# Performance work log

Measured on AMD Instinct MI355X. Metric: run time of the kernel, lower is better.

## Reference

```python
import jax, jax.numpy as jnp
import numpy as np

N_NODES = 50000
N_EDGES = 600000
NUM_RELS = 5
IN_CH = 768
HID = 128
OUT_CH = 128
REL_DIM = 200


def _segment_softmax(scores, seg, n):
    # numerically stable softmax over variable-size segments (destination nodes)
    m = jax.ops.segment_max(scores, seg, num_segments=n)
    e = jnp.exp(scores - m[seg])
    s = jax.ops.segment_sum(e, seg, num_segments=n)
    return e / s[seg]


def _hgn_conv(x, edge_index, edge_type, W, Wr, a, Wres, rel_tab, final):
    # x: [N, h_in]; W: [h, h_in]; Wr: [h, rel_dim]; a: [3h]; rel_tab: [R, rel_dim]
    src = edge_index[0]
    dst = edge_index[1]
    n = x.shape[0]
    h = W.shape[0]
    Wx = x @ W.T                      # [N, h] (shared by x_i, x_j, messages)
    rel = rel_tab[edge_type] @ Wr.T   # [E, h]
    aA, aB, aC = a[:h], a[h:2 * h], a[2 * h:]
    # a([Wx_i | Wx_j | Wr rel]) decomposed to avoid materializing the concat
    score = Wx[dst] @ aA + Wx[src] @ aB + rel @ aC   # [E]
    alpha = jax.nn.leaky_relu(score, 0.2)
    alpha = _segment_softmax(alpha, dst, n)
    agg = jax.ops.segment_sum(Wx[src] * alpha[:, None], dst, num_segments=n)
    out = jax.nn.elu(agg + x @ Wres.T)
    if final:
        out = out / jnp.maximum(jnp.linalg.norm(out, axis=1, keepdims=True), 1e-12)
    return out, alpha


def setup_inputs() -> dict:
    key = jax.random.key(0)
    ks = jax.random.split(key, 20)
    s = 0.02
    return {
        "x": jax.random.normal(ks[0], (N_NODES, IN_CH), jnp.float32),
        "edge_index": jax.random.randint(ks[1], (2, N_EDGES), 0, N_NODES, jnp.int64 if jax.config.jax_enable_x64 else jnp.int32),
        "edge_type": jax.random.randint(ks[2], (N_EDGES,), 0, NUM_RELS, jnp.int64 if jax.config.jax_enable_x64 else jnp.int32),
        "l1_W": jax.random.normal(ks[3], (HID, IN_CH), jnp.float32) * s,
        "l1_b": jnp.zeros((HID,), jnp.float32),
        "l2_W": jax.random.normal(ks[4], (OUT_CH, HID), jnp.float32) * s,
        "l2_b": jnp.zeros((OUT_CH,), jnp.float32),
        "W1": jax.random.normal(ks[5], (HID, HID), jnp.float32) * s,
        "Wr1": jax.random.normal(ks[6], (HID, REL_DIM), jnp.float32) * s,
        "a1": jax.random.normal(ks[7], (3 * HID,), jnp.float32) * s,
        "Wres1": jax.random.normal(ks[8], (HID, HID), jnp.float32) * s,
        "rel1": jax.random.normal(ks[9], (NUM_RELS, REL_DIM), jnp.float32),
        "W2": jax.random.normal(ks[10], (HID, HID), jnp.float32) * s,
        "Wr2": jax.random.normal(ks[11], (HID, REL_DIM), jnp.float32) * s,
        "a2": jax.random.normal(ks[12], (3 * HID,), jnp.float32) * s,
        "Wres2": jax.random.normal(ks[13], (HID, HID), jnp.float32) * s,
        "rel2": jax.random.normal(ks[14], (NUM_RELS, REL_DIM), jnp.float32),
    }


def reference(x, edge_index, edge_type, l1_W, l1_b, l2_W, l2_b,
              W1, Wr1, a1, Wres1, rel1, W2, Wr2, a2, Wres2, rel2):
    out = jax.nn.leaky_relu(x @ l1_W.T + l1_b, 0.01)
    # layer 1 (dropout is identity in eval mode)
    out, alpha = _hgn_conv(out, edge_index, edge_type, W1, Wr1, a1, Wres1, rel1, final=False)
    # layer 2: original code blends alpha into self.alpha but weights messages
    # with its own (unblended) softmax alpha, so pre_alpha does not affect output
    out, _ = _hgn_conv(out, edge_index, edge_type, W2, Wr2, a2, Wres2, rel2, final=True)
    out = jax.nn.leaky_relu(out @ l2_W.T + l2_b, 0.01)
    return out
```

## Files before the change

### kernel.cpp

```cpp
#include <hip/hip_runtime.h>

namespace {

typedef unsigned short ushort_t;
typedef unsigned int uint_t;
typedef __attribute__((ext_vector_type(8))) short bf16x8;
typedef __attribute__((ext_vector_type(4))) float f32x4;

constexpr int N   = 50000;
constexpr int E   = 600000;
constexpr int NR  = 5;
constexpr int KIN = 768;
constexpr int H   = 128;
constexpr int RD  = 200;

__device__ inline ushort_t f2b(float f){
  uint_t u = __builtin_bit_cast(uint_t, f);
  uint_t r = (u + 0x7FFFu + ((u >> 16) & 1u)) >> 16;
  return (ushort_t)r;
}
__device__ inline float b2f_lo(uint_t u){ return __builtin_bit_cast(float, u << 16); }
__device__ inline float b2f_hi(uint_t u){ return __builtin_bit_cast(float, u & 0xFFFF0000u); }
__device__ inline float b2f_us(ushort_t h){ return __builtin_bit_cast(float, ((uint_t)h) << 16); }
__device__ inline uint_t cvtpk(float lo, float hi){
  uint_t r;
  asm("v_cvt_pk_bf16_f32 %0, %1, %2" : "=v"(r) : "v"(lo), "v"(hi));
  return r;
}

__global__ void prep_k(const float* __restrict__ l1W, const float* __restrict__ W1,
                       const float* __restrict__ R1, const float* __restrict__ W2,
                       const float* __restrict__ R2, const float* __restrict__ l2W,
                       ushort_t* __restrict__ wts, int* __restrict__ deg,
                       const float* __restrict__ rel1, const float* __restrict__ Wr1,
                       const float* __restrict__ a1, float* __restrict__ sC1,
                       const float* __restrict__ rel2, const float* __restrict__ Wr2,
                       const float* __restrict__ a2, float* __restrict__ sC2){
  constexpr int S0 = H * KIN;
  constexpr int S1 = H * H;
  int b = blockIdx.x, tid = threadIdx.x;
  if (b < 704){
    int i = b * 256 + tid;
    float v;
    if (i < S0) v = l1W[i];
    else {
      int j = i - S0, seg = j >> 14, off = j & (S1 - 1);
      const float* srcs[5] = {W1, R1, W2, R2, l2W};
      v = srcs[seg][off];
    }
    wts[i] = f2b(v);
  } else if (b < 900){
    int i = (b - 704) * 256 + tid;
    if (i < N) deg[i] = 0;
  } else {
    int L = b - 900;
    const float* rel = L ? rel2 : rel1;
    const float* Wr  = L ? Wr2  : Wr1;
    const float* a   = L ? a2   : a1;
    float*       sC  = L ? sC2  : sC1;
    __shared__ float red[256];
    int n = tid >> 1, half = tid & 1;
    float aC = a[256 + n];
    for (int r = 0; r < NR; ++r){
      float p = 0.f;
      for (int k = half * 100; k < half * 100 + 100; ++k)
        p += rel[r * RD + k] * Wr[n * RD + k];
      red[tid] = p * aC;
      __syncthreads();
      for (int s = 128; s > 0; s >>= 1){
        if (tid < s) red[tid] += red[tid + s];
        __syncthreads();
      }
      if (tid == 0) sC[r] = red[0];
      __syncthreads();
    }
  }
}

__global__ void degcount_k(const int* __restrict__ dst, int* __restrict__ deg){
  int e = blockIdx.x * 256 + threadIdx.x;
  if (e < E) atomicAdd(&deg[dst[e]], 1);
}

__global__ void scan1_k(const int* __restrict__ deg, int* __restrict__ chunk,
                        int* __restrict__ bsums, int n){
  __shared__ int s[256];
  int tid = threadIdx.x, i = blockIdx.x * 256 + tid;
  int v = (i < n) ? deg[i] : 0;
  s[tid] = v; __syncthreads();
  for (int off = 1; off < 256; off <<= 1){
    int t = (tid >= off) ? s[tid - off] : 0;
    __syncthreads();
    s[tid] += t;
    __syncthreads();
  }
  if (i < n) chunk[i] = s[tid] - v;
  if (tid == 255) bsums[blockIdx.x] = s[255];
}

__global__ void scan2_k(const int* __restrict__ bsums, int* __restrict__ boffs, int nb){
  __shared__ int s[256];
  int tid = threadIdx.x;
  int v = (tid < nb) ? bsums[tid] : 0;
  s[tid] = v; __syncthreads();
  for (int off = 1; off < 256; off <<= 1){
    int t = (tid >= off) ? s[tid - off] : 0;
    __syncthreads();
    s[tid] += t;
    __syncthreads();
  }
  if (tid < nb) boffs[tid] = s[tid] - v;
}

__global__ void scan3_k(int* __restrict__ rowptr, const int* __restrict__ boffs,
                        int* __restrict__ cursor, int n, int total){
  int i = blockIdx.x * 256 + threadIdx.x;
  if (i < n){
    int v = rowptr[i] + boffs[blockIdx.x];
    rowptr[i] = v; cursor[i] = v;
  }
  if (i == 0) rowptr[n] = total;
}

__global__ void fill_k(const int* __restrict__ src, const int* __restrict__ dst,
                       const int* __restrict__ et, int* __restrict__ cursor,
                       int* __restrict__ cpk){
  int e = blockIdx.x * 256 + threadIdx.x;
  if (e < E){
    int d = dst[e];
    int p = atomicAdd(&cursor[d], 1);
    cpk[p] = src[e] | (et[e] << 16);
  }
}

template<int K1, int M1, bool AFP32, bool NORM, bool STORE1, int M2>
__global__ __launch_bounds__(256, 3) void gfused_k(
    const void* __restrict__ Ap, const ushort_t* __restrict__ Wb1,
    const float* __restrict__ bias1, const ushort_t* __restrict__ aggM,
    ushort_t* __restrict__ out1,
    const ushort_t* __restrict__ Wb2, const float* __restrict__ vec2,
    void* __restrict__ out2, float* __restrict__ sA, float* __restrict__ sB, int M)
{
  __shared__ __align__(16) ushort_t Cs[64 * 128];
  const int tid  = threadIdx.x;
  const int wave = tid >> 6, lane = tid & 63;
  const int l15  = lane & 15, quad = lane >> 4;
  const int row0 = blockIdx.x * 64;
  const int arow_l = wave * 16 + l15;
  int ar = row0 + arow_l; if (ar >= M) ar = M - 1;

  f32x4 acc[8];
  #pragma unroll
  for (int t = 0; t < 8; ++t) acc[t] = (f32x4){0.f, 0.f, 0.f, 0.f};

  const ushort_t* wb = Wb1 + (size_t)l15 * K1 + quad * 8;
  if (AFP32){
    const float* ap = (const float*)Ap + (size_t)ar * K1 + quad * 8;
    #pragma unroll 2
    for (int k0 = 0; k0 < K1; k0 += 32){
      float4 u0 = *reinterpret_cast<const float4*>(ap + k0);
      float4 u1 = *reinterpret_cast<const float4*>(ap + k0 + 4);
      uint4 av;
      av.x = cvtpk(u0.x, u0.y); av.y = cvtpk(u0.z, u0.w);
      av.z = cvtpk(u1.x, u1.y); av.w = cvtpk(u1.z, u1.w);
      bf16x8 af = __builtin_bit_cast(bf16x8, av);
      #pragma unroll
      for (int t = 0; t < 8; ++t){
        bf16x8 bfr = *reinterpret_cast<const bf16x8*>(wb + (size_t)t * 16 * K1 + k0);
        acc[t] = __builtin_amdgcn_mfma_f32_16x16x32_bf16(af, bfr, acc[t], 0, 0, 0);
      }
    }
  } else {
    const ushort_t* apb = (const ushort_t*)Ap + (size_t)ar * K1 + quad * 8;
    #pragma unroll 2
    for (int k0 = 0; k0 < K1; k0 += 32){
      bf16x8 af = *reinterpret_cast<const bf16x8*>(apb + k0);
      #pragma unroll
      for (int t = 0; t < 8; ++t){
        bf16x8 bfr = *reinterpret_cast<const bf16x8*>(wb + (size_t)t * 16 * K1 + k0);
        acc[t] = __builtin_amdgcn_mfma_f32_16x16x32_bf16(af, bfr, acc[t], 0, 0, 0);
      }
    }
  }

  const int lr0 = wave * 16 + quad * 4;
  float vv[8][4];
  #pragma unroll
  for (int t = 0; t < 8; ++t){
    #pragma unroll
    for (int r = 0; r < 4; ++r){
      int col = t * 16 + l15;
      float v = acc[t][r];
      if (M1 == 1){
        v += bias1[col];
        v = v > 0.f ? v : 0.01f * v;
      } else {
        int g = row0 + lr0 + r;
        float ag = (g < M) ? b2f_us(aggM[(size_t)g * 128 + col]) : 0.f;
        v += ag;
        v = v > 0.f ? v : __expf(v) - 1.f;
      }
      vv[t][r] = v;
    }
  }
  if (NORM){
    #pragma unroll
    for (int r = 0; r < 4; ++r){
      float ss = 0.f;
      #pragma unroll
      for (int t = 0; t < 8; ++t) ss += vv[t][r] * vv[t][r];
      #pragma unroll
      for (int off = 1; off < 16; off <<= 1) ss += __shfl_xor(ss, off, 64);
      float sc = 1.f / fmaxf(sqrtf(ss), 1e-12f);
      #pragma unroll
      for (int t = 0; t < 8; ++t) vv[t][r] *= sc;
    }
  }
  #pragma unroll
  for (int t = 0; t < 8; t += 2){
    #pragma unroll
    for (int r = 0; r < 4; ++r){
      int row = lr0 + r;
      int key = row & 7;
      uint_t pr = cvtpk(vv[t][r], vv[t + 1][r]);
      int c0 = t * 16 + l15, c1 = c0 + 16;
      int p0 = ((c0 >> 3) ^ key) << 3, p1 = ((c1 >> 3) ^ key) << 3;
      Cs[row * 128 + p0 + (l15 & 7)] = (ushort_t)pr;
      Cs[row * 128 + p1 + (l15 & 7)] = (ushort_t)(pr >> 16);
      if (STORE1){
        int g = row0 + row;
        if (g < M){
          out1[(size_t)g * 128 + c0] = (ushort_t)pr;
          out1[(size_t)g * 128 + c1] = (ushort_t)(pr >> 16);
        }
      }
    }
  }
  __syncthreads();

  #pragma unroll
  for (int t = 0; t < 8; ++t) acc[t] = (f32x4){0.f, 0.f, 0.f, 0.f};
  {
    const int rr   = wave * 16 + l15;
    const int rkey = l15 & 7;
    const ushort_t* w2 = Wb2 + (size_t)l15 * 128 + quad * 8;
    #pragma unroll 2
    for (int kk = 0; kk < 4; ++kk){
      int ph = (((kk * 4 + quad) ^ rkey) << 3);
      bf16x8 af2 = *reinterpret_cast<const bf16x8*>(&Cs[rr * 128 + ph]);
      #pragma unroll
      for (int t = 0; t < 8; ++t){
        bf16x8 bfr = *reinterpret_cast<const bf16x8*>(w2 + (size_t)t * 16 * 128 + kk * 32);
        acc[t] = __builtin_amdgcn_mfma_f32_16x16x32_bf16(af2, bfr, acc[t], 0, 0, 0);
      }
    }
  }

  if (M2 == 1){
    #pragma unroll
    for (int t = 0; t < 8; ++t){
      #pragma unroll
      for (int r = 0; r < 4; ++r){
        int grow = row0 + lr0 + r;
        if (grow >= M) continue;
        int col = t * 16 + l15;
        float v = acc[t][r] + vec2[col];
        v = v > 0.f ? v : 0.01f * v;
        ((float*)out2)[(size_t)grow * 128 + col] = v;
      }
    }
  } else {
    #pragma unroll
    for (int t = 0; t < 8; t += 2){
      #pragma unroll
      for (int r = 0; r < 4; ++r){
        int grow = row0 + lr0 + r;
        if (grow >= M) continue;
        int c0 = t * 16 + l15;
        uint_t pr = cvtpk(acc[t][r], acc[t + 1][r]);
        ((ushort_t*)out2)[(size_t)grow * 128 + c0]      = (ushort_t)pr;
        ((ushort_t*)out2)[(size_t)grow * 128 + c0 + 16] = (ushort_t)(pr >> 16);
      }
    }
    #pragma unroll
    for (int r = 0; r < 4; ++r){
      float pa = 0.f, pb = 0.f;
      #pragma unroll
      for (int t = 0; t < 8; ++t){
        int col = t * 16 + l15;
        pa += acc[t][r] * vec2[col];
        pb += acc[t][r] * vec2[128 + col];
      }
      #pragma unroll
      for (int off = 1; off < 16; off <<= 1){
        pa += __shfl_xor(pa, off, 64);
        pb += __shfl_xor(pb, off, 64);
      }
      int grow = row0 + lr0 + r;
      if (l15 == r && grow < M){ sA[grow] = pa; sB[grow] = pb; }
    }
  }
}

__global__ __launch_bounds__(256) void agg_k(
    const ushort_t* __restrict__ Wx, const float* __restrict__ sA,
    const float* __restrict__ sB, const float* __restrict__ sC,
    const int* __restrict__ rowptr, const int* __restrict__ cpk,
    uint_t* __restrict__ aggU, int n)
{
  const int node  = blockIdx.x * 16 + (threadIdx.x >> 4);
  const int l     = threadIdx.x & 15;
  const int gbase = threadIdx.x & 48;
  if (node >= n) return;
  int p0 = rowptr[node], p1 = rowptr[node + 1];
  int deg = p1 - p0;
  float sa = sA[node];
  float m = -1e30f, ssum = 0.f;
  float a[8];
  #pragma unroll
  for (int j = 0; j < 8; ++j) a[j] = 0.f;

  for (int c0 = 0; c0 < deg; c0 += 16){
    int cnt = deg - c0; if (cnt > 16) cnt = 16;
    bool ok = l < cnt;
    int pk = cpk[p0 + c0 + (ok ? l : 0)];
    float s = sa + sB[pk & 0xFFFF] + sC[pk >> 16];
    s = s > 0.f ? s : 0.2f * s;
    float sv = ok ? s : -1e30f;
    #pragma unroll
    for (int off = 8; off > 0; off >>= 1) sv = fmaxf(sv, __shfl_xor(sv, off, 16));
    float mn = fmaxf(m, sv);
    float corr = __expf(m - mn);
    ssum *= corr;
    #pragma unroll
    for (int j = 0; j < 8; ++j) a[j] *= corr;
    float ev = ok ? __expf(s - mn) : 0.f;
    float es = ev;
    #pragma unroll
    for (int off = 8; off > 0; off >>= 1) es += __shfl_xor(es, off, 16);
    ssum += es;
    m = mn;
    int png = ok ? pk : 0;

    for (int e = 0; e < cnt; e += 4){
      int b0l = gbase + e;
      int pe0 = __shfl(png, b0l,     64), pe1 = __shfl(png, b0l + 1, 64);
      int pe2 = __shfl(png, b0l + 2, 64), pe3 = __shfl(png, b0l + 3, 64);
      float e0 = __shfl(ev, b0l,     64), e1 = __shfl(ev, b0l + 1, 64);
      float e2 = __shfl(ev, b0l + 2, 64), e3 = __shfl(ev, b0l + 3, 64);
      uint4 u0 = *reinterpret_cast<const uint4*>(Wx + (size_t)(pe0 & 0xFFFF) * 128 + l * 8);
      uint4 u1 = *reinterpret_cast<const uint4*>(Wx + (size_t)(pe1 & 0xFFFF) * 128 + l * 8);
      uint4 u2 = *reinterpret_cast<const uint4*>(Wx + (size_t)(pe2 & 0xFFFF) * 128 + l * 8);
      uint4 u3 = *reinterpret_cast<const uint4*>(Wx + (size_t)(pe3 & 0xFFFF) * 128 + l * 8);
      a[0] += e0 * b2f_lo(u0.x); a[1] += e0 * b2f_hi(u0.x);
      a[2] += e0 * b2f_lo(u0.y); a[3] += e0 * b2f_hi(u0.y);
      a[4] += e0 * b2f_lo(u0.z); a[5] += e0 * b2f_hi(u0.z);
      a[6] += e0 * b2f_lo(u0.w); a[7] += e0 * b2f_hi(u0.w);
      a[0] += e1 * b2f_lo(u1.x); a[1] += e1 * b2f_hi(u1.x);
      a[2] += e1 * b2f_lo(u1.y); a[3] += e1 * b2f_hi(u1.y);
      a[4] += e1 * b2f_lo(u1.z); a[5] += e1 * b2f_hi(u1.z);
      a[6] += e1 * b2f_lo(u1.w); a[7] += e1 * b2f_hi(u1.w);
      a[0] += e2 * b2f_lo(u2.x); a[1] += e2 * b2f_hi(u2.x);
      a[2] += e2 * b2f_lo(u2.y); a[3] += e2 * b2f_hi(u2.y);
      a[4] += e2 * b2f_lo(u2.z); a[5] += e2 * b2f_hi(u2.z);
      a[6] += e2 * b2f_lo(u2.w); a[7] += e2 * b2f_hi(u2.w);
      a[0] += e3 * b2f_lo(u3.x); a[1] += e3 * b2f_hi(u3.x);
      a[2] += e3 * b2f_lo(u3.y); a[3] += e3 * b2f_hi(u3.y);
      a[4] += e3 * b2f_lo(u3.z); a[5] += e3 * b2f_hi(u3.z);
      a[6] += e3 * b2f_lo(u3.w); a[7] += e3 * b2f_hi(u3.w);
    }
  }
  float inv = (deg > 0) ? 1.f / ssum : 0.f;
  uint4 o;
  o.x = cvtpk(a[0] * inv, a[1] * inv);
  o.y = cvtpk(a[2] * inv, a[3] * inv);
  o.z = cvtpk(a[4] * inv, a[5] * inv);
  o.w = cvtpk(a[6] * inv, a[7] * inv);
  *reinterpret_cast<uint4*>(aggU + (size_t)node * 64 + l * 4) = o;
}

}

extern "C" void kernel_launch(void* const* d_in, const int* in_sizes, int n_in,
                              void* d_out, int out_size, void* d_ws, size_t ws_size,
                              hipStream_t stream)
{
  const float* x     = (const float*)d_in[0];
  const int*   eidx  = (const int*)d_in[1];
  const int*   et    = (const int*)d_in[2];
  const float* l1W   = (const float*)d_in[3];
  const float* l1b   = (const float*)d_in[4];
  const float* l2W   = (const float*)d_in[5];
  const float* l2b   = (const float*)d_in[6];
  const float* W1    = (const float*)d_in[7];
  const float* Wr1   = (const float*)d_in[8];
  const float* a1    = (const float*)d_in[9];
  const float* Wres1 = (const float*)d_in[10];
  const float* rel1  = (const float*)d_in[11];
  const float* W2    = (const float*)d_in[12];
  const float* Wr2   = (const float*)d_in[13];
  const float* a2    = (const float*)d_in[14];
  const float* Wres2 = (const float*)d_in[15];
  const float* rel2  = (const float*)d_in[16];
  float* outp = (float*)d_out;

  const int* esrc = eidx;
  const int* edst = eidx + E;

  float* f = (float*)d_ws;
  size_t o = 0;
  float* sA   = f + o; o += N;
  float* sB   = f + o; o += N;
  float* sC1  = f + o; o += 8;
  float* sC2  = f + o; o += 8;
  ushort_t* us = (ushort_t*)(f + o);
  size_t ou = 0;
  ushort_t* b0   = us + ou; ou += (size_t)N * H;
  ushort_t* b1   = us + ou; ou += (size_t)N * H;
  ushort_t* Wxb  = us + ou; ou += (size_t)N * H;
  ushort_t* aggB = us + ou; ou += (size_t)N * H;
  ushort_t* wtsb = us + ou; ou += (size_t)H * KIN + 5 * H * H;
  ushort_t* l1Wb = wtsb;
  ushort_t* W1b  = wtsb + H * KIN;
  ushort_t* R1b  = W1b + H * H;
  ushort_t* W2b  = R1b + H * H;
  ushort_t* R2b  = W2b + H * H;
  ushort_t* l2Wb = R2b + H * H;
  if (ou & 1) ou += 1;
  int* wi = (int*)(us + ou);
  size_t oi = 0;
  int* deg    = wi + oi; oi += N;
  int* rowptr = wi + oi; oi += N + 1;
  int* cursor = wi + oi; oi += N;
  int* bsums  = wi + oi; oi += 256;
  int* boffs  = wi + oi; oi += 256;
  int* cpk    = wi + oi; oi += E;

  const int EB    = (E + 255) / 256;
  const int NB256 = (N + 255) / 256;
  const int GB    = (N + 63) / 64;
  const int NB16  = (N + 15) / 16;

  prep_k<<<902, 256, 0, stream>>>(l1W, W1, Wres1, W2, Wres2, l2W, wtsb, deg,
                                  rel1, Wr1, a1, sC1, rel2, Wr2, a2, sC2);
  degcount_k<<<EB, 256, 0, stream>>>(edst, deg);
  scan1_k<<<NB256, 256, 0, stream>>>(deg, rowptr, bsums, N);
  scan2_k<<<1, 256, 0, stream>>>(bsums, boffs, NB256);
  scan3_k<<<NB256, 256, 0, stream>>>(rowptr, boffs, cursor, N, E);
  fill_k<<<EB, 256, 0, stream>>>(esrc, edst, et, cursor, cpk);

  gfused_k<KIN, 1, true, false, true, 3><<<GB, 256, 0, stream>>>(
      x, l1Wb, l1b, nullptr, b0, W1b, a1, Wxb, sA, sB, N);
  agg_k<<<NB16, 256, 0, stream>>>(Wxb, sA, sB, sC1, rowptr, cpk, (uint_t*)aggB, N);

  gfused_k<H, 2, false, false, true, 3><<<GB, 256, 0, stream>>>(
      b0, R1b, nullptr, aggB, b1, W2b, a2, Wxb, sA, sB, N);
  agg_k<<<NB16, 256, 0, stream>>>(Wxb, sA, sB, sC2, rowptr, cpk, (uint_t*)aggB, N);

  gfused_k<H, 2, false, true, false, 1><<<GB, 256, 0, stream>>>(
      b1, R2b, nullptr, aggB, nullptr, l2Wb, l2b, outp, nullptr, nullptr, N);
}
```

Before: 575.2 us.

## Stage GEMM A/B tiles through LDS with async global_load_lds pipelining

Rewrites the first GEMM main loop in the fused kernel. Instead of every wave loading A and B fragments straight from global memory, the A tiles are double-buffered in LDS (converted to bf16 on the way in) and the weight B tiles are triple-buffered in LDS using global_load_lds, with explicit vmcnt waits and barriers so loads overlap the MFMAs. It also stages the aggregated aggM tile into LDS with coalesced 16-byte loads instead of scattered 2-byte reads. The costs are more LDS per block, which may limit occupancy at 3 blocks per CU, and hand-tuned waitcnt logic that is fragile.

```diff
diff --git a/kernel.cpp b/kernel.cpp
--- a/kernel.cpp
+++ b/kernel.cpp
@@ -26,6 +26,18 @@
   uint_t r;
   asm("v_cvt_pk_bf16_f32 %0, %1, %2" : "=v"(r) : "v"(lo), "v"(hi));
   return r;
+}
+
+typedef __attribute__((address_space(1))) const unsigned int glb_u32;
+typedef __attribute__((address_space(3))) unsigned int lds_u32;
+__device__ __forceinline__ void glds16(const void* g, void* l){
+  __builtin_amdgcn_global_load_lds((glb_u32*)g, (lds_u32*)l, 16, 0, 0);
+}
+template<int Nn> __device__ __forceinline__ void wait_vmcnt(){
+  asm volatile("s_waitcnt vmcnt(%0)" :: "n"(Nn) : "memory");
+}
+__device__ __forceinline__ void wait_lgkm0(){
+  asm volatile("s_waitcnt lgkmcnt(0)" ::: "memory");
 }
 
 __global__ void prep_k(const float* __restrict__ l1W, const float* __restrict__ W1,
@@ -141,46 +153,109 @@
     const ushort_t* __restrict__ Wb2, const float* __restrict__ vec2,
     void* __restrict__ out2, float* __restrict__ sA, float* __restrict__ sB, int M)
 {
+  constexpr int NT = K1 / 32;
+  constexpr int AI = AFP32 ? 2 : 1;
+  __shared__ __align__(16) ushort_t Abuf[2][64 * 32];
+  __shared__ __align__(16) ushort_t Bbuf[3][128 * 32];
   __shared__ __align__(16) ushort_t Cs[64 * 128];
   const int tid  = threadIdx.x;
   const int wave = tid >> 6, lane = tid & 63;
   const int l15  = lane & 15, quad = lane >> 4;
   const int row0 = blockIdx.x * 64;
-  const int arow_l = wave * 16 + l15;
-  int ar = row0 + arow_l; if (ar >= M) ar = M - 1;
+
+  int arow_ld = row0 + (tid >> 2); if (arow_ld >= M) arow_ld = M - 1;
+  const int aoff  = (tid & 3) * 8;
+  const int awoff = (tid >> 2) * 32 + aoff;
+  const int c0 = wave * 2, c1 = wave * 2 + 1;
+  const ushort_t* bsrc0 = Wb1 + (size_t)(c0 * 16 + (lane >> 2)) * K1 + (lane & 3) * 8;
+  const ushort_t* bsrc1 = bsrc0 + (size_t)16 * K1;
+
+#define ISSUE_A(d0, d1, kk) do{                                               \
+    if constexpr (AFP32){                                                     \
+      const float* ap_ = (const float*)Ap + (size_t)arow_ld * K1 + (kk) + aoff; \
+      d0 = *reinterpret_cast<const uint4*>(ap_);                              \
+      d1 = *reinterpret_cast<const uint4*>(ap_ + 4);                          \
+    } else {                                                                  \
+      d0 = *reinterpret_cast<const uint4*>(                                   \
+          (const ushort_t*)Ap + (size_t)arow_ld * K1 + (kk) + aoff);          \
+    } }while(0)
+
+#define WRITE_A(bi, s0, s1) do{ uint4 av_;                                    \
+    if constexpr (AFP32){                                                     \
+      float4 f0_ = __builtin_bit_cast(float4, s0);                            \
+      float4 f1_ = __builtin_bit_cast(float4, s1);                            \
+      av_.x = cvtpk(f0_.x, f0_.y); av_.y = cvtpk(f0_.z, f0_.w);               \
+      av_.z = cvtpk(f1_.x, f1_.y); av_.w = cvtpk(f1_.z, f1_.w);               \
+    } else av_ = s0;                                                          \
+    *reinterpret_cast<uint4*>(&Abuf[bi][awoff]) = av_; }while(0)
+
+#define ISSUE_B(bi, kk) do{                                                   \
+    glds16(bsrc0 + (kk), &Bbuf[bi][c0 * 512]);                                \
+    glds16(bsrc1 + (kk), &Bbuf[bi][c1 * 512]); }while(0)
+
+#define KSTEP(ab, bb) do{                                                     \
+    bf16x8 af_ = *reinterpret_cast<const bf16x8*>(                            \
+        &Abuf[ab][(wave * 16 + l15) * 32 + quad * 8]);                        \
+    _Pragma("unroll")                                                         \
+    for (int t_ = 0; t_ < 8; ++t_){                                           \
+      bf16x8 bf_ = *reinterpret_cast<const bf16x8*>(                          \
+          &Bbuf[bb][(t_ * 16 + l15) * 32 + quad * 8]);                        \
+      acc[t_] = __builtin_amdgcn_mfma_f32_16x16x32_bf16(af_, bf_, acc[t_], 0, 0, 0); \
+    } }while(0)
 
   f32x4 acc[8];
   #pragma unroll
   for (int t = 0; t < 8; ++t) acc[t] = (f32x4){0.f, 0.f, 0.f, 0.f};
 
-  const ushort_t* wb = Wb1 + (size_t)l15 * K1 + quad * 8;
-  if (AFP32){
-    const float* ap = (const float*)Ap + (size_t)ar * K1 + quad * 8;
-    #pragma unroll 2
-    for (int k0 = 0; k0 < K1; k0 += 32){
-      float4 u0 = *reinterpret_cast<const float4*>(ap + k0);
-      float4 u1 = *reinterpret_cast<const float4*>(ap + k0 + 4);
-      uint4 av;
-      av.x = cvtpk(u0.x, u0.y); av.y = cvtpk(u0.z, u0.w);
-      av.z = cvtpk(u1.x, u1.y); av.w = cvtpk(u1.z, u1.w);
-      bf16x8 af = __builtin_bit_cast(bf16x8, av);
-      #pragma unroll
-      for (int t = 0; t < 8; ++t){
-        bf16x8 bfr = *reinterpret_cast<const bf16x8*>(wb + (size_t)t * 16 * K1 + k0);
-        acc[t] = __builtin_amdgcn_mfma_f32_16x16x32_bf16(af, bfr, acc[t], 0, 0, 0);
-      }
-    }
-  } else {
-    const ushort_t* apb = (const ushort_t*)Ap + (size_t)ar * K1 + quad * 8;
-    #pragma unroll 2
-    for (int k0 = 0; k0 < K1; k0 += 32){
-      bf16x8 af = *reinterpret_cast<const bf16x8*>(apb + k0);
-      #pragma unroll
-      for (int t = 0; t < 8; ++t){
-        bf16x8 bfr = *reinterpret_cast<const bf16x8*>(wb + (size_t)t * 16 * K1 + k0);
-        acc[t] = __builtin_amdgcn_mfma_f32_16x16x32_bf16(af, bfr, acc[t], 0, 0, 0);
-      }
-    }
+  uint4 pa0_0, pa0_1, pa1_0, pa1_1;
+  ISSUE_A(pa0_0, pa0_1, 0);
+  ISSUE_B(0, 0);
+  ISSUE_A(pa1_0, pa1_1, 32);
+  ISSUE_B(1, 32);
+  wait_vmcnt<AI + 4>();
+  WRITE_A(0, pa0_0, pa0_1);
+  wait_lgkm0();
+  __builtin_amdgcn_s_barrier();
+
+  int bt = 0;
+  for (int t = 0; t < NT; t += 2){
+    wait_vmcnt<AI + 2>();
+    KSTEP(0, bt);
+    wait_vmcnt<2>();
+    WRITE_A(1, pa1_0, pa1_1);
+    { int b2 = bt + 2; if (b2 >= 3) b2 -= 3;
+      if (t + 2 < NT){ ISSUE_A(pa0_0, pa0_1, (t + 2) * 32); ISSUE_B(b2, (t + 2) * 32); } }
+    wait_lgkm0();
+    __builtin_amdgcn_s_barrier();
+    bt = (bt >= 2) ? 0 : bt + 1;
+    wait_vmcnt<AI + 2>();
+    KSTEP(1, bt);
+    if (t + 2 < NT){
+      wait_vmcnt<2>();
+      WRITE_A(0, pa0_0, pa0_1);
+    }
+    { int b2 = bt + 2; if (b2 >= 3) b2 -= 3;
+      if (t + 3 < NT){ ISSUE_A(pa1_0, pa1_1, (t + 3) * 32); ISSUE_B(b2, (t + 3) * 32); } }
+    wait_lgkm0();
+    __builtin_amdgcn_s_barrier();
+    bt = (bt >= 2) ? 0 : bt + 1;
+  }
+#undef ISSUE_A
+#undef WRITE_A
+#undef ISSUE_B
+#undef KSTEP
+
+  ushort_t* Ag = &Bbuf[0][0];
+  if (M1 == 2){
+    #pragma unroll
+    for (int i = 0; i < 4; ++i){
+      int idx = tid + 256 * i, r = idx >> 4, c8 = idx & 15;
+      int g = row0 + r;
+      uint4 v = make_uint4(0, 0, 0, 0);
+      if (g < M) v = *reinterpret_cast<const uint4*>(aggM + (size_t)g * 128 + c8 * 8);
+      *reinterpret_cast<uint4*>(&Ag[r * 128 + c8 * 8]) = v;
+    }
+    __syncthreads();
   }
 
   const int lr0 = wave * 16 + quad * 4;
@@ -195,9 +270,7 @@
         v += bias1[col];
         v = v > 0.f ? v : 0.01f * v;
       } else {
-        int g = row0 + lr0 + r;
-        float ag = (g < M) ? b2f_us(aggM[(size_t)g * 128 + col]) : 0.f;
-        v += ag;
+        v += b2f_us(Ag[(lr0 + r) * 128 + col]);
         v = v > 0.f ? v : __expf(v) - 1.f;
       }
       vv[t][r] = v;
@@ -223,15 +296,15 @@
       int row = lr0 + r;
       int key = row & 7;
       uint_t pr = cvtpk(vv[t][r], vv[t + 1][r]);
-      int c0 = t * 16 + l15, c1 = c0 + 16;
-      int p0 = ((c0 >> 3) ^ key) << 3, p1 = ((c1 >> 3) ^ key) << 3;
+      int c0s = t * 16 + l15, c1s = c0s + 16;
+      int p0 = ((c0s >> 3) ^ key) << 3, p1 = ((c1s >> 3) ^ key) << 3;
       Cs[row * 128 + p0 + (l15 & 7)] = (ushort_t)pr;
       Cs[row * 128 + p1 + (l15 & 7)] = (ushort_t)(pr >> 16);
       if (STORE1){
         int g = row0 + row;
         if (g < M){
-          out1[(size_t)g * 128 + c0] = (ushort_t)pr;
-          out1[(size_t)g * 128 + c1] = (ushort_t)(pr >> 16);
+          out1[(size_t)g * 128 + c0s] = (ushort_t)pr;
+          out1[(size_t)g * 128 + c1s] = (ushort_t)(pr >> 16);
         }
       }
     }
@@ -276,10 +349,10 @@
       for (int r = 0; r < 4; ++r){
         int grow = row0 + lr0 + r;
         if (grow >= M) continue;
-        int c0 = t * 16 + l15;
+        int c0s = t * 16 + l15;
         uint_t pr = cvtpk(acc[t][r], acc[t + 1][r]);
-        ((ushort_t*)out2)[(size_t)grow * 128 + c0]      = (ushort_t)pr;
-        ((ushort_t*)out2)[(size_t)grow * 128 + c0 + 16] = (ushort_t)(pr >> 16);
+        ((ushort_t*)out2)[(size_t)grow * 128 + c0s]      = (ushort_t)pr;
+        ((ushort_t*)out2)[(size_t)grow * 128 + c0s + 16] = (ushort_t)(pr >> 16);
       }
     }
     #pragma unroll
```

After: 524.1 us. 8.9% less time.

## Stage GEMM tiles in LDS with register prefetch and 2x2 wave split

Applied to the files above, without the earlier changes.

The fused GEMM kernel now processes 32-row blocks split across a 2x2 wave grid, each wave computing 16 rows by 64 columns. A and W tiles are staged through padded shared memory with a one-step register prefetch, instead of each wave reading W fragments straight from global memory. The aggregate input is preloaded into shared memory, and the norm and score reductions are combined across the two column-waves through a small shared buffer. Launch bounds allow higher occupancy, at the cost of two barriers per K step and twice as many blocks.

```diff
diff --git a/kernel.cpp b/kernel.cpp
--- a/kernel.cpp
+++ b/kernel.cpp
@@ -134,70 +134,92 @@
 }
 
 template<int K1, int M1, bool AFP32, bool NORM, bool STORE1, int M2>
-__global__ __launch_bounds__(256, 3) void gfused_k(
+__global__ __launch_bounds__(256, 6) void gfused_k(
     const void* __restrict__ Ap, const ushort_t* __restrict__ Wb1,
     const float* __restrict__ bias1, const ushort_t* __restrict__ aggM,
     ushort_t* __restrict__ out1,
     const ushort_t* __restrict__ Wb2, const float* __restrict__ vec2,
     void* __restrict__ out2, float* __restrict__ sA, float* __restrict__ sB, int M)
 {
-  __shared__ __align__(16) ushort_t Cs[64 * 128];
+  constexpr int AP = 40;
+  constexpr int BP = 40;
+  constexpr int CP = 136;
+  __shared__ __align__(16) ushort_t As[32 * AP];
+  __shared__ __align__(16) ushort_t Bs[128 * BP];
+  __shared__ __align__(16) ushort_t Cs[32 * CP];
+  __shared__ float cmb[2][32][2];
   const int tid  = threadIdx.x;
   const int wave = tid >> 6, lane = tid & 63;
   const int l15  = lane & 15, quad = lane >> 4;
-  const int row0 = blockIdx.x * 64;
-  const int arow_l = wave * 16 + l15;
-  int ar = row0 + arow_l; if (ar >= M) ar = M - 1;
-
-  f32x4 acc[8];
+  const int wr   = wave >> 1, wc = wave & 1;
+  const int row0 = blockIdx.x * 32;
+
+  if (M1 == 2){
+    #pragma unroll
+    for (int i = 0; i < 2; ++i){
+      int idx = tid + 256 * i;
+      int r = idx >> 4, c8 = idx & 15;
+      int g = row0 + r;
+      uint4 v = make_uint4(0, 0, 0, 0);
+      if (g < M) v = *reinterpret_cast<const uint4*>(aggM + (size_t)g * 128 + c8 * 8);
+      *reinterpret_cast<uint4*>(&Cs[r * CP + c8 * 8]) = v;
+    }
+  }
+
+  f32x4 acc[4];
   #pragma unroll
-  for (int t = 0; t < 8; ++t) acc[t] = (f32x4){0.f, 0.f, 0.f, 0.f};
-
-  const ushort_t* wb = Wb1 + (size_t)l15 * K1 + quad * 8;
-  if (AFP32){
-    const float* ap = (const float*)Ap + (size_t)ar * K1 + quad * 8;
-    #pragma unroll 2
-    for (int k0 = 0; k0 < K1; k0 += 32){
-      float4 u0 = *reinterpret_cast<const float4*>(ap + k0);
-      float4 u1 = *reinterpret_cast<const float4*>(ap + k0 + 4);
-      uint4 av;
-      av.x = cvtpk(u0.x, u0.y); av.y = cvtpk(u0.z, u0.w);
-      av.z = cvtpk(u1.x, u1.y); av.w = cvtpk(u1.z, u1.w);
-      bf16x8 af = __builtin_bit_cast(bf16x8, av);
-      #pragma unroll
-      for (int t = 0; t < 8; ++t){
-        bf16x8 bfr = *reinterpret_cast<const bf16x8*>(wb + (size_t)t * 16 * K1 + k0);
-        acc[t] = __builtin_amdgcn_mfma_f32_16x16x32_bf16(af, bfr, acc[t], 0, 0, 0);
-      }
-    }
-  } else {
-    const ushort_t* apb = (const ushort_t*)Ap + (size_t)ar * K1 + quad * 8;
-    #pragma unroll 2
-    for (int k0 = 0; k0 < K1; k0 += 32){
-      bf16x8 af = *reinterpret_cast<const bf16x8*>(apb + k0);
-      #pragma unroll
-      for (int t = 0; t < 8; ++t){
-        bf16x8 bfr = *reinterpret_cast<const bf16x8*>(wb + (size_t)t * 16 * K1 + k0);
-        acc[t] = __builtin_amdgcn_mfma_f32_16x16x32_bf16(af, bfr, acc[t], 0, 0, 0);
-      }
-    }
-  }
-
-  const int lr0 = wave * 16 + quad * 4;
-  float vv[8][4];
+  for (int t = 0; t < 4; ++t) acc[t] = (f32x4){0.f, 0.f, 0.f, 0.f};
+
+  const int arow_s = tid >> 3, aseg = tid & 7;
+  int agrow = row0 + arow_s; if (agrow >= M) agrow = M - 1;
+  const int awoff = arow_s * AP + aseg * 4;
+  const int bn = tid >> 1, bs16 = (tid & 1) * 16;
+  const ushort_t* bsrc = Wb1 + (size_t)bn * K1 + bs16;
+
+  float4 pfa; uint2 pua; uint4 pb0, pb1;
+  if (AFP32) pfa = *reinterpret_cast<const float4*>((const float*)Ap + (size_t)agrow * K1 + aseg * 4);
+  else       pua = *reinterpret_cast<const uint2*>((const ushort_t*)Ap + (size_t)agrow * K1 + aseg * 4);
+  pb0 = *reinterpret_cast<const uint4*>(bsrc);
+  pb1 = *reinterpret_cast<const uint4*>(bsrc + 8);
+
+  for (int k0 = 0; k0 < K1; k0 += 32){
+    { uint2 w;
+      if (AFP32){ w.x = cvtpk(pfa.x, pfa.y); w.y = cvtpk(pfa.z, pfa.w); }
+      else w = pua;
+      *reinterpret_cast<uint2*>(&As[awoff]) = w;
+      *reinterpret_cast<uint4*>(&Bs[bn * BP + bs16])     = pb0;
+      *reinterpret_cast<uint4*>(&Bs[bn * BP + bs16 + 8]) = pb1;
+    }
+    __syncthreads();
+    if (k0 + 32 < K1){
+      const int k1 = k0 + 32;
+      if (AFP32) pfa = *reinterpret_cast<const float4*>((const float*)Ap + (size_t)agrow * K1 + k1 + aseg * 4);
+      else       pua = *reinterpret_cast<const uint2*>((const ushort_t*)Ap + (size_t)agrow * K1 + k1 + aseg * 4);
+      pb0 = *reinterpret_cast<const uint4*>(bsrc + k1);
+      pb1 = *reinterpret_cast<const uint4*>(bsrc + k1 + 8);
+    }
+    bf16x8 af = *reinterpret_cast<const bf16x8*>(&As[(wr * 16 + l15) * AP + quad * 8]);
+    #pragma unroll
+    for (int t = 0; t < 4; ++t){
+      bf16x8 bfr = *reinterpret_cast<const bf16x8*>(&Bs[(wc * 64 + t * 16 + l15) * BP + quad * 8]);
+      acc[t] = __builtin_amdgcn_mfma_f32_16x16x32_bf16(af, bfr, acc[t], 0, 0, 0);
+    }
+    __syncthreads();
+  }
+
+  const int lr0 = wr * 16 + quad * 4;
+  float vv[4][4];
   #pragma unroll
-  for (int t = 0; t < 8; ++t){
+  for (int t = 0; t < 4; ++t){
     #pragma unroll
     for (int r = 0; r < 4; ++r){
-      int col = t * 16 + l15;
+      int col = wc * 64 + t * 16 + l15;
       float v = acc[t][r];
       if (M1 == 1){
         v += bias1[col];
         v = v > 0.f ? v : 0.01f * v;
       } else {
-        int g = row0 + lr0 + r;
-        float ag = (g < M) ? b2f_us(aggM[(size_t)g * 128 + col]) : 0.f;
-        v += ag;
+        v += b2f_us(Cs[(lr0 + r) * CP + col]);
         v = v > 0.f ? v : __expf(v) - 1.f;
       }
       vv[t][r] = v;
@@ -208,25 +230,29 @@
     for (int r = 0; r < 4; ++r){
       float ss = 0.f;
       #pragma unroll
-      for (int t = 0; t < 8; ++t) ss += vv[t][r] * vv[t][r];
+      for (int t = 0; t < 4; ++t) ss += vv[t][r] * vv[t][r];
       #pragma unroll
       for (int off = 1; off < 16; off <<= 1) ss += __shfl_xor(ss, off, 64);
-      float sc = 1.f / fmaxf(sqrtf(ss), 1e-12f);
-      #pragma unroll
-      for (int t = 0; t < 8; ++t) vv[t][r] *= sc;
+      if (l15 == 0) cmb[wc][lr0 + r][0] = ss;
+    }
+    __syncthreads();
+    #pragma unroll
+    for (int r = 0; r < 4; ++r){
+      float tot = cmb[0][lr0 + r][0] + cmb[1][lr0 + r][0];
+      float sc = 1.f / fmaxf(sqrtf(tot), 1e-12f);
+      #pragma unroll
+      for (int t = 0; t < 4; ++t) vv[t][r] *= sc;
     }
   }
   #pragma unroll
-  for (int t = 0; t < 8; t += 2){
+  for (int t = 0; t < 4; t += 2){
     #pragma unroll
     for (int r = 0; r < 4; ++r){
       int row = lr0 + r;
-      int key = row & 7;
+      int c0 = wc * 64 + t * 16 + l15, c1 = c0 + 16;
       uint_t pr = cvtpk(vv[t][r], vv[t + 1][r]);
-      int c0 = t * 16 + l15, c1 = c0 + 16;
-      int p0 = ((c0 >> 3) ^ key) << 3, p1 = ((c1 >> 3) ^ key) << 3;
-      Cs[row * 128 + p0 + (l15 & 7)] = (ushort_t)pr;
-      Cs[row * 128 + p1 + (l15 & 7)] = (ushort_t)(pr >> 16);
+      Cs[row * CP + c0] = (ushort_t)pr;
+      Cs[row * CP + c1] = (ushort_t)(pr >> 16);
       if (STORE1){
         int g = row0 + row;
         if (g < M){
@@ -239,17 +265,15 @@
   __syncthreads();
 
   #pragma unroll
-  for (int t = 0; t < 8; ++t) acc[t] = (f32x4){0.f, 0.f, 0.f, 0.f};
+  for (int t = 0; t < 4; ++t) acc[t] = (f32x4){0.f, 0.f, 0.f, 0.f};
   {
-    const int rr   = wave * 16 + l15;
-    const int rkey = l15 & 7;
-    const ushort_t* w2 = Wb2 + (size_t)l15 * 128 + quad * 8;
-    #pragma unroll 2
+    const int rr = wr * 16 + l15;
+    const ushort_t* w2 = Wb2 + (size_t)(wc * 64 + l15) * 128 + quad * 8;
+    #pragma unroll
     for (int kk = 0; kk < 4; ++kk){
-      int ph = (((kk * 4 + quad) ^ rkey) << 3);
-      bf16x8 af2 = *reinterpret_cast<const bf16x8*>(&Cs[rr * 128 + ph]);
-      #pragma unroll
-      for (int t = 0; t < 8; ++t){
+      bf16x8 af2 = *reinterpret_cast<const bf16x8*>(&Cs[rr * CP + kk * 32 + quad * 8]);
+      #pragma unroll
+      for (int t = 0; t < 4; ++t){
         bf16x8 bfr = *reinterpret_cast<const bf16x8*>(w2 + (size_t)t * 16 * 128 + kk * 32);
         acc[t] = __builtin_amdgcn_mfma_f32_16x16x32_bf16(af2, bfr, acc[t], 0, 0, 0);
       }
@@ -258,12 +282,12 @@
 
   if (M2 == 1){
     #pragma unroll
-    for (int t = 0; t < 8; ++t){
+    for (int t = 0; t < 4; ++t){
       #pragma unroll
       for (int r = 0; r < 4; ++r){
         int grow = row0 + lr0 + r;
         if (grow >= M) continue;
-        int col = t * 16 + l15;
+        int col = wc * 64 + t * 16 + l15;
         float v = acc[t][r] + vec2[col];
         v = v > 0.f ? v : 0.01f * v;
         ((float*)out2)[(size_t)grow * 128 + col] = v;
@@ -271,12 +295,12 @@
     }
   } else {
     #pragma unroll
-    for (int t = 0; t < 8; t += 2){
+    for (int t = 0; t < 4; t += 2){
       #pragma unroll
       for (int r = 0; r < 4; ++r){
         int grow = row0 + lr0 + r;
         if (grow >= M) continue;
-        int c0 = t * 16 + l15;
+        int c0 = wc * 64 + t * 16 + l15;
         uint_t pr = cvtpk(acc[t][r], acc[t + 1][r]);
         ((ushort_t*)out2)[(size_t)grow * 128 + c0]      = (ushort_t)pr;
         ((ushort_t*)out2)[(size_t)grow * 128 + c0 + 16] = (ushort_t)(pr >> 16);
@@ -286,8 +310,8 @@
     for (int r = 0; r < 4; ++r){
       float pa = 0.f, pb = 0.f;
       #pragma unroll
-      for (int t = 0; t < 8; ++t){
-        int col = t * 16 + l15;
+      for (int t = 0; t < 4; ++t){
+        int col = wc * 64 + t * 16 + l15;
         pa += acc[t][r] * vec2[col];
         pb += acc[t][r] * vec2[128 + col];
       }
@@ -296,8 +320,14 @@
         pa += __shfl_xor(pa, off, 64);
         pb += __shfl_xor(pb, off, 64);
       }
-      int grow = row0 + lr0 + r;
-      if (l15 == r && grow < M){ sA[grow] = pa; sB[grow] = pb; }
+      if (l15 == 0){ cmb[wc][lr0 + r][0] = pa; cmb[wc][lr0 + r][1] = pb; }
+    }
+    __syncthreads();
+    if (tid < 64){
+      int row = tid >> 1, ab = tid & 1;
+      float v = cmb[0][row][ab] + cmb[1][row][ab];
+      int g = row0 + row;
+      if (g < M){ if (ab) sB[g] = v; else sA[g] = v; }
     }
   }
 }
@@ -438,7 +468,7 @@
 
   const int EB    = (E + 255) / 256;
   const int NB256 = (N + 255) / 256;
-  const int GB    = (N + 63) / 64;
+  const int GB    = (N + 31) / 32;
   const int NB16  = (N + 15) / 16;
 
   prep_k<<<902, 256, 0, stream>>>(l1W, W1, Wres1, W2, Wres2, l2W, wtsb, deg,
```

After: 516.1 us. 10.3% less time.
